# Optimization experiments

Measured on AMD Instinct MI355X. Metric: run time of the kernel, lower is better.

The kernel has to match this reference:

```python
import jax, jax.numpy as jnp
import numpy as np

# Surrogate-gradient Heaviside spike (original repo uses @jax.custom_vjp spike_fn;
# forward is a hard step, backward uses a fast-sigmoid surrogate scaled by alpha).
@jax.custom_vjp
def spike_fn(x, alpha):
    return jnp.where(x > 0, 1.0, 0.0).astype(x.dtype)

def _spike_fwd(x, alpha):
    return spike_fn(x, alpha), (x, alpha)

def _spike_bwd(res, g):
    x, alpha = res
    surr = 1.0 / (alpha * jnp.abs(x) + 1.0) ** 2  # fast-sigmoid surrogate
    return (g * surr, jnp.zeros_like(alpha))

spike_fn.defvjp(_spike_fwd, _spike_bwd)


def setup_inputs() -> dict:
    key = jax.random.key(0)
    k1, k2 = jax.random.split(key)
    B, T, H, W, F = 8, 64, 16, 16, 256
    x = jax.random.normal(k1, (B, T, H, W, F), dtype=jnp.float32)
    w_rec = jax.random.normal(k2, (F, F), dtype=jnp.float32) * 0.05  # normal(stddev=0.05) init
    return {
        "x": x,
        "w_rec": w_rec,
        "hp_alif_d": jnp.float32(0.7),
        "hp_alif_adp": jnp.float32(0.9),
        "hp_alif_beta": jnp.float32(1.8),
        "hp_alpha": jnp.float32(2.0),
    }


def reference(x, w_rec, hp_alif_d, hp_alif_adp, hp_alif_beta, hp_alpha):
    # x: (B, T, H, W, F) -> time-major (T, B, H, W, F)
    x_seq = jnp.moveaxis(x, 1, 0)

    def scan_fn(carry, x_t):
        v, theta, prev_s = carry
        theta_next = theta * hp_alif_adp + prev_s * hp_alif_beta
        rec_input = jnp.dot(prev_s, w_rec)  # contract last (feature) dim
        v_next = v * hp_alif_d + x_t + rec_input
        vth_t = 0.5 + theta_next
        s = spike_fn(v_next - vth_t, hp_alpha)
        v_next = v_next - jax.lax.stop_gradient(s) * vth_t
        return (v_next, theta_next, s), s

    z = jnp.zeros_like(x_seq[0])
    _, spikes = jax.lax.scan(scan_fn, (z, z, z), x_seq)
    return jnp.moveaxis(spikes, 0, 1)  # back to (B, T, H, W, F)
```

## Files before the change

### kernel.cpp

```cpp
#include <hip/hip_runtime.h>


#define FDIM 256
#define TSTEPS 64
#define HWDIM 256

__global__ __launch_bounds__(256, 8) void alif_kernel(
    const float* __restrict__ x,
    const float* __restrict__ w_rec,
    const float* __restrict__ hp_d_p,
    const float* __restrict__ hp_adp_p,
    const float* __restrict__ hp_beta_p,
    float* __restrict__ out)
{
    const int tid  = threadIdx.x;
    const int blk  = blockIdx.x;
    const int wave = tid >> 6;
    const int lane = tid & 63;

    const float d    = hp_d_p[0];
    const float adp  = hp_adp_p[0];
    const float beta = hp_beta_p[0];

    __shared__ int list[FDIM];
    __shared__ unsigned long long wmask[4];

    const int b  = blk >> 8;
    const int hw = blk & 255;
    size_t idx = (size_t)b * TSTEPS * (HWDIM * FDIM) + (size_t)hw * FDIM + tid;
    const size_t tstride = (size_t)HWDIM * FDIM;

    const float* wcol = w_rec + tid;

    float v = 0.f, th = 0.f, s = 0.f;

    for (int t = 0; t < TSTEPS; ++t) {
        float xt = x[idx];

        unsigned long long m = __ballot(s != 0.f);
        if (lane == 0) wmask[wave] = m;
        __syncthreads();
        int base = 0, total = 0;
        #pragma unroll
        for (int w = 0; w < 4; ++w) {
            int c = __popcll(wmask[w]);
            if (w < wave) base += c;
            total += c;
        }
        if (s != 0.f) {
            int pos = base + __popcll(m & ((1ull << lane) - 1ull));
            list[pos] = tid;
        }
        __syncthreads();

        float rec = 0.f;
        for (int i = 0; i < total; ++i) {
            int k = list[i];
            rec += wcol[(size_t)k << 8];
        }

        th = fmaf(th, adp, s * beta);
        float vn  = fmaf(v, d, xt) + rec;
        float vth = 0.5f + th;
        float sn  = (vn - vth) > 0.f ? 1.f : 0.f;
        v = vn - sn * vth;
        s = sn;
        out[idx] = sn;

        idx += tstride;
        __syncthreads();
    }
}

extern "C" void kernel_launch(void* const* d_in, const int* in_sizes, int n_in,
                              void* d_out, int out_size, void* d_ws, size_t ws_size,
                              hipStream_t stream) {
    const float* x     = (const float*)d_in[0];
    const float* w_rec = (const float*)d_in[1];
    const float* hp_d  = (const float*)d_in[2];
    const float* hp_adp  = (const float*)d_in[3];
    const float* hp_beta = (const float*)d_in[4];
    float* out = (float*)d_out;

    alif_kernel<<<2048, 256, 0, stream>>>(x, w_rec, hp_d, hp_adp, hp_beta, out);
}
```

Measured before the change: 386.6 us.

## Map one wave per site with float4 features and cache half of w_rec in LDS

Each wavefront now owns a whole (b,hw) site, with each lane handling four features as float4. Block-wide barriers and the shared spike list are replaced by a shuffle/readlane spike bitmask built inside the wave. The first 128 rows of w_rec are staged in 128KB of LDS and the remaining rows are read from global memory, and the next timestep's x is prefetched. The grid shrinks to 256 blocks of 512 threads, one block per CU, which lowers occupancy and relies on LDS capacity and L2 hits for the global half of the weights.

```diff
diff --git a/kernel.cpp b/kernel.cpp
--- a/kernel.cpp
+++ b/kernel.cpp
@@ -1,11 +1,21 @@
 #include <hip/hip_runtime.h>
 
 
-#define FDIM 256
 #define TSTEPS 64
-#define HWDIM 256
+typedef unsigned long long u64;
 
-__global__ __launch_bounds__(256, 8) void alif_kernel(
+__device__ __forceinline__ u64 rl64(u64 v, int srcLane) {
+    unsigned lo = __builtin_amdgcn_readlane((unsigned)v, srcLane);
+    unsigned hi = __builtin_amdgcn_readlane((unsigned)(v >> 32), srcLane);
+    return (((u64)hi) << 32) | lo;
+}
+
+__device__ __forceinline__ int nextbit(u64& w0, u64& w1) {
+    if (w0) { int i = (int)__builtin_ctzll(w0); w0 &= w0 - 1ull; return i; }
+    int i = (int)__builtin_ctzll(w1); w1 &= w1 - 1ull; return 64 + i;
+}
+
+__global__ __launch_bounds__(512) void alif_kernel(
     const float* __restrict__ x,
     const float* __restrict__ w_rec,
     const float* __restrict__ hp_d_p,
@@ -14,73 +24,154 @@
     float* __restrict__ out)
 {
     const int tid  = threadIdx.x;
-    const int blk  = blockIdx.x;
+    const int lane = tid & 63;
     const int wave = tid >> 6;
-    const int lane = tid & 63;
+    const int site = (int)(blockIdx.x << 3) | wave;
+    const int b  = site >> 8;
+    const int hw = site & 255;
 
     const float d    = hp_d_p[0];
     const float adp  = hp_adp_p[0];
     const float beta = hp_beta_p[0];
 
-    __shared__ int list[FDIM];
-    __shared__ unsigned long long wmask[4];
+    __shared__ float lw[32768];
 
-    const int b  = blk >> 8;
-    const int hw = blk & 255;
-    size_t idx = (size_t)b * TSTEPS * (HWDIM * FDIM) + (size_t)hw * FDIM + tid;
-    const size_t tstride = (size_t)HWDIM * FDIM;
+    {
+        const float4* src = (const float4*)w_rec;
+        float4* dst = (float4*)lw;
+        #pragma unroll
+        for (int i = 0; i < 16; ++i) dst[i * 512 + tid] = src[i * 512 + tid];
+    }
+    __syncthreads();
 
-    const float* wcol = w_rec + tid;
+    size_t xidx = (size_t)b * ((size_t)TSTEPS * 65536) + (size_t)hw * 256
+                + ((size_t)lane << 2);
+    const int lof  = lane << 2;
+    const int fb16 = lane << 4;
+    const char* wg = ((const char*)w_rec) + (128 << 10);
 
-    float v = 0.f, th = 0.f, s = 0.f;
+    float4 v  = make_float4(0.f, 0.f, 0.f, 0.f);
+    float4 th = make_float4(0.f, 0.f, 0.f, 0.f);
+    float4 s  = make_float4(0.f, 0.f, 0.f, 0.f);
+    float4 xt = *(const float4*)(x + xidx);
+
+#define LROW(k) (*(const float4*)(lw + ((k) << 8) + lof))
+#define GROW(k) (*(const float4*)(wg + (((size_t)(k)) << 10) + fb16))
+#define ACC(q)  do { rec.x += (q).x; rec.y += (q).y; rec.z += (q).z; rec.w += (q).w; } while (0)
 
     for (int t = 0; t < TSTEPS; ++t) {
-        float xt = x[idx];
+        unsigned nib = (s.x != 0.f ? 1u : 0u) | (s.y != 0.f ? 2u : 0u)
+                     | (s.z != 0.f ? 4u : 0u) | (s.w != 0.f ? 8u : 0u);
+        u64 val = ((u64)nib) << ((lane & 15) << 2);
+        val |= __shfl_xor(val, 1);
+        val |= __shfl_xor(val, 2);
+        val |= __shfl_xor(val, 4);
+        val |= __shfl_xor(val, 8);
+        u64 M0 = rl64(val, 0),  M1 = rl64(val, 16);
+        u64 M2 = rl64(val, 32), M3 = rl64(val, 48);
 
-        unsigned long long m = __ballot(s != 0.f);
-        if (lane == 0) wmask[wave] = m;
-        __syncthreads();
-        int base = 0, total = 0;
-        #pragma unroll
-        for (int w = 0; w < 4; ++w) {
-            int c = __popcll(wmask[w]);
-            if (w < wave) base += c;
-            total += c;
-        }
-        if (s != 0.f) {
-            int pos = base + __popcll(m & ((1ull << lane) - 1ull));
-            list[pos] = tid;
-        }
-        __syncthreads();
+        size_t nidx = xidx + (t < TSTEPS - 1 ? (size_t)65536 : (size_t)0);
+        float4 xn = *(const float4*)(x + nidx);
 
-        float rec = 0.f;
-        for (int i = 0; i < total; ++i) {
-            int k = list[i];
-            rec += wcol[(size_t)k << 8];
+        float4 rec = make_float4(0.f, 0.f, 0.f, 0.f);
+
+        {
+            u64 a = M0, c = M1;
+            int cnt = (int)__popcll(a) + (int)__popcll(c);
+            while (cnt >= 8) {
+                int k0 = nextbit(a, c); int k1 = nextbit(a, c);
+                int k2 = nextbit(a, c); int k3 = nextbit(a, c);
+                int k4 = nextbit(a, c); int k5 = nextbit(a, c);
+                int k6 = nextbit(a, c); int k7 = nextbit(a, c);
+                float4 q0 = LROW(k0), q1 = LROW(k1), q2 = LROW(k2), q3 = LROW(k3);
+                float4 q4 = LROW(k4), q5 = LROW(k5), q6 = LROW(k6), q7 = LROW(k7);
+                ACC(q0); ACC(q1); ACC(q2); ACC(q3);
+                ACC(q4); ACC(q5); ACC(q6); ACC(q7);
+                cnt -= 8;
+            }
+            if (cnt & 4) {
+                int k0 = nextbit(a, c); int k1 = nextbit(a, c);
+                int k2 = nextbit(a, c); int k3 = nextbit(a, c);
+                float4 q0 = LROW(k0), q1 = LROW(k1), q2 = LROW(k2), q3 = LROW(k3);
+                ACC(q0); ACC(q1); ACC(q2); ACC(q3);
+            }
+            if (cnt & 2) {
+                int k0 = nextbit(a, c); int k1 = nextbit(a, c);
+                float4 q0 = LROW(k0), q1 = LROW(k1);
+                ACC(q0); ACC(q1);
+            }
+            if (cnt & 1) {
+                int k0 = nextbit(a, c);
+                float4 q0 = LROW(k0);
+                ACC(q0);
+            }
         }
 
-        th = fmaf(th, adp, s * beta);
-        float vn  = fmaf(v, d, xt) + rec;
-        float vth = 0.5f + th;
-        float sn  = (vn - vth) > 0.f ? 1.f : 0.f;
-        v = vn - sn * vth;
+        {
+            u64 a = M2, c = M3;
+            int cnt = (int)__popcll(a) + (int)__popcll(c);
+            while (cnt >= 8) {
+                int k0 = nextbit(a, c); int k1 = nextbit(a, c);
+                int k2 = nextbit(a, c); int k3 = nextbit(a, c);
+                int k4 = nextbit(a, c); int k5 = nextbit(a, c);
+                int k6 = nextbit(a, c); int k7 = nextbit(a, c);
+                float4 q0 = GROW(k0), q1 = GROW(k1), q2 = GROW(k2), q3 = GROW(k3);
+                float4 q4 = GROW(k4), q5 = GROW(k5), q6 = GROW(k6), q7 = GROW(k7);
+                ACC(q0); ACC(q1); ACC(q2); ACC(q3);
+                ACC(q4); ACC(q5); ACC(q6); ACC(q7);
+                cnt -= 8;
+            }
+            if (cnt & 4) {
+                int k0 = nextbit(a, c); int k1 = nextbit(a, c);
+                int k2 = nextbit(a, c); int k3 = nextbit(a, c);
+                float4 q0 = GROW(k0), q1 = GROW(k1), q2 = GROW(k2), q3 = GROW(k3);
+                ACC(q0); ACC(q1); ACC(q2); ACC(q3);
+            }
+            if (cnt & 2) {
+                int k0 = nextbit(a, c); int k1 = nextbit(a, c);
+                float4 q0 = GROW(k0), q1 = GROW(k1);
+                ACC(q0); ACC(q1);
+            }
+            if (cnt & 1) {
+                int k0 = nextbit(a, c);
+                float4 q0 = GROW(k0);
+                ACC(q0);
+            }
+        }
+
+        float4 sn;
+        th.x = fmaf(th.x, adp, s.x * beta);
+        { float vn = fmaf(v.x, d, xt.x) + rec.x; float vt = 0.5f + th.x;
+          sn.x = (vn - vt) > 0.f ? 1.f : 0.f; v.x = vn - sn.x * vt; }
+        th.y = fmaf(th.y, adp, s.y * beta);
+        { float vn = fmaf(v.y, d, xt.y) + rec.y; float vt = 0.5f + th.y;
+          sn.y = (vn - vt) > 0.f ? 1.f : 0.f; v.y = vn - sn.y * vt; }
+        th.z = fmaf(th.z, adp, s.z * beta);
+        { float vn = fmaf(v.z, d, xt.z) + rec.z; float vt = 0.5f + th.z;
+          sn.z = (vn - vt) > 0.f ? 1.f : 0.f; v.z = vn - sn.z * vt; }
+        th.w = fmaf(th.w, adp, s.w * beta);
+        { float vn = fmaf(v.w, d, xt.w) + rec.w; float vt = 0.5f + th.w;
+          sn.w = (vn - vt) > 0.f ? 1.f : 0.f; v.w = vn - sn.w * vt; }
         s = sn;
-        out[idx] = sn;
+        *(float4*)(out + xidx) = s;
 
-        idx += tstride;
-        __syncthreads();
+        xidx = nidx;
+        xt = xn;
     }
+#undef LROW
+#undef GROW
+#undef ACC
 }
 
 extern "C" void kernel_launch(void* const* d_in, const int* in_sizes, int n_in,
                               void* d_out, int out_size, void* d_ws, size_t ws_size,
                               hipStream_t stream) {
-    const float* x     = (const float*)d_in[0];
-    const float* w_rec = (const float*)d_in[1];
-    const float* hp_d  = (const float*)d_in[2];
+    const float* x       = (const float*)d_in[0];
+    const float* w_rec   = (const float*)d_in[1];
+    const float* hp_d    = (const float*)d_in[2];
     const float* hp_adp  = (const float*)d_in[3];
     const float* hp_beta = (const float*)d_in[4];
     float* out = (float*)d_out;
 
-    alif_kernel<<<2048, 256, 0, stream>>>(x, w_rec, hp_d, hp_adp, hp_beta, out);
+    alif_kernel<<<256, 512, 0, stream>>>(x, w_rec, hp_d, hp_adp, hp_beta, out);
 }
```

After: 329.7 us. -14.7%, faster.
